# Optimization experiments

Hardware: AMD Instinct MI355X
Metric: run time of the kernel (lower is better)

## Reference

```python
import jax, jax.numpy as jnp
import numpy as np

N = 100000      # nodes
E = 1600000     # edges (avg degree 16)
IN, HID, OUT = 256, 256, 128


def setup_inputs() -> dict:
    key = jax.random.key(0)
    ks = jax.random.split(key, 9)
    x = jax.random.normal(ks[0], (N, IN), jnp.float32)
    edge_index = jax.random.randint(ks[1], (2, E), 0, N, dtype=jnp.int64)
    perm = jax.random.permutation(ks[2], N).astype(jnp.int64)
    # GCN layer params (glorot-ish scale) and Bilinear discriminator params
    W1 = jax.random.normal(ks[3], (IN, HID), jnp.float32) * (1.0 / np.sqrt(IN))
    b1 = jnp.zeros((HID,), jnp.float32)
    W2 = jax.random.normal(ks[4], (HID, OUT), jnp.float32) * (1.0 / np.sqrt(HID))
    b2 = jnp.zeros((OUT,), jnp.float32)
    Wb = jax.random.normal(ks[5], (OUT, OUT), jnp.float32) * (1.0 / np.sqrt(OUT))
    bb = jnp.zeros((1,), jnp.float32)
    return {"x": x, "edge_index": edge_index, "perm": perm,
            "W1": W1, "b1": b1, "W2": W2, "b2": b2, "Wb": Wb, "bb": bb}


def reference(x, edge_index, perm, W1, b1, W2, b2, Wb, bb):
    n = x.shape[0]
    src, dst = edge_index[0], edge_index[1]
    # GCN symmetric norm with self-loops: deg = 1 + in-degree
    deg = 1.0 + jax.ops.segment_sum(jnp.ones(src.shape[0], x.dtype), dst,
                                    num_segments=n)
    dinv = jax.lax.rsqrt(deg)                 # [N]
    enorm = dinv[src] * dinv[dst]             # per-edge norm
    self_norm = dinv * dinv                   # self-loop norm

    def gcn(h, W, b):
        hw = h @ W                                            # [N, F]
        agg = jax.ops.segment_sum(hw[src] * enorm[:, None], dst,
                                  num_segments=n)             # scatter-add
        return agg + self_norm[:, None] * hw + b

    def encode(h):
        return gcn(jax.nn.relu(gcn(h, W1, b1)), W2, b2)       # [N, OUT]

    H = encode(x)
    s = jax.nn.sigmoid(H.mean(axis=0))                        # summary [OUT]

    def disc(Hh):
        # nn.Bilinear(d, d, 1): score_n = H_n^T Wb s + bb
        return (jnp.einsum('nd,de,e->n', Hh, Wb, s) + bb)[:, None]

    pos_scores = disc(H)
    neg_scores = disc(encode(x[perm]))
    return pos_scores, neg_scores
```

## Files before the change

kernel.cpp:

```cpp
#include <hip/hip_runtime.h>


typedef __attribute__((ext_vector_type(8))) short bh8;
typedef __attribute__((ext_vector_type(4))) float f4;
typedef __attribute__((ext_vector_type(4))) unsigned short u16x4;

#define AS1 __attribute__((address_space(1)))
#define AS3 __attribute__((address_space(3)))

__device__ __forceinline__ unsigned short f2b(float f) {
    unsigned int u = __float_as_uint(f);
    unsigned int r = (u + 0x7FFFu + ((u >> 16) & 1u)) >> 16;
    return (unsigned short)r;
}
__device__ __forceinline__ float b2f(unsigned short h) {
    return __uint_as_float(((unsigned int)h) << 16);
}

__global__ void k_degree(const int* __restrict__ dst, int* __restrict__ deg, int E) {
    int e = blockIdx.x * blockDim.x + threadIdx.x;
    if (e < E) atomicAdd(&deg[dst[e]], 1);
}

__global__ void k_dinv(const int* __restrict__ deg, float* __restrict__ dinv,
                       int* __restrict__ rowptr, int N, int E) {
    int n = blockIdx.x * blockDim.x + threadIdx.x;
    if (n < N) dinv[n] = 1.0f / sqrtf(1.0f + (float)deg[n]);
    if (n == 0) rowptr[N] = E;
}

__global__ void k_scanA(const int* __restrict__ in, int* __restrict__ out,
                        int* __restrict__ bsum, int n) {
    __shared__ int sh[256];
    int t = threadIdx.x;
    int base = blockIdx.x * 1024 + t * 4;
    int v[4];
#pragma unroll
    for (int j = 0; j < 4; ++j) v[j] = (base + j < n) ? in[base + j] : 0;
    int s = v[0] + v[1] + v[2] + v[3];
    sh[t] = s;
    __syncthreads();
    for (int off = 1; off < 256; off <<= 1) {
        int u = (t >= off) ? sh[t - off] : 0;
        __syncthreads();
        sh[t] += u;
        __syncthreads();
    }
    int excl = sh[t] - s;
    if (t == 255) bsum[blockIdx.x] = sh[255];
    int run = excl;
#pragma unroll
    for (int j = 0; j < 4; ++j) {
        if (base + j < n) out[base + j] = run;
        run += v[j];
    }
}

__global__ void k_scanB(const int* __restrict__ bsum, int* __restrict__ boff, int nb) {
    __shared__ int sh[128];
    int t = threadIdx.x;
    int v = (t < nb) ? bsum[t] : 0;
    sh[t] = v;
    __syncthreads();
    for (int off = 1; off < 128; off <<= 1) {
        int u = (t >= off) ? sh[t - off] : 0;
        __syncthreads();
        sh[t] += u;
        __syncthreads();
    }
    boff[t] = sh[t] - v;
}

__global__ void k_scanC(int* __restrict__ out, const int* __restrict__ boff, int n) {
    int t = threadIdx.x;
    int base = blockIdx.x * 1024 + t * 4;
    int add = boff[blockIdx.x];
#pragma unroll
    for (int j = 0; j < 4; ++j)
        if (base + j < n) out[base + j] += add;
}

__global__ void k_fill(const int* __restrict__ src, const int* __restrict__ dst,
                       const int* __restrict__ rowptr, int* __restrict__ cursor,
                       int* __restrict__ csr, int E) {
    int e = blockIdx.x * blockDim.x + threadIdx.x;
    if (e >= E) return;
    int d = dst[e];
    int p = rowptr[d] + atomicAdd(&cursor[d], 1);
    csr[p] = src[e];
}

__global__ void k_split(const float* __restrict__ in, unsigned short* __restrict__ hi,
                        unsigned short* __restrict__ lo, long n4) {
    long i = (long)blockIdx.x * blockDim.x + threadIdx.x;
    if (i >= n4) return;
    float4 v = ((const float4*)in)[i];
    float f[4] = {v.x, v.y, v.z, v.w};
    u16x4 h, l;
#pragma unroll
    for (int j = 0; j < 4; ++j) {
        unsigned short hb = f2b(f[j]);
        h[j] = hb;
        l[j] = f2b(f[j] - b2f(hb));
    }
    ((u16x4*)hi)[i] = h;
    ((u16x4*)lo)[i] = l;
}

__global__ void k_wsplitT(const float* __restrict__ W, unsigned short* __restrict__ thi,
                          unsigned short* __restrict__ tlo, int K, int Nc) {
    int t = blockIdx.x * blockDim.x + threadIdx.x;
    if (t >= K * Nc) return;
    int k = t / Nc, n = t % Nc;
    float f = W[t];
    unsigned short hb = f2b(f);
    thi[n * K + k] = hb;
    tlo[n * K + k] = f2b(f - b2f(hb));
}

__global__ __launch_bounds__(256, 2) void k_gemm_mfma(
        const unsigned short* __restrict__ Ahi, const unsigned short* __restrict__ Alo,
        const unsigned short* __restrict__ Bhi, const unsigned short* __restrict__ Blo,
        unsigned short* __restrict__ C, int M, int K, int Nc) {
    __shared__ short lds[4][128 * 32];
    const int tid  = threadIdx.x;
    const int lane = tid & 63;
    const int w    = tid >> 6;
    const int wr   = w >> 1, wc = w & 1;
    const int row0 = blockIdx.y * 128;
    const int col0 = blockIdx.x * 128;

    const unsigned short* sp = (w == 0) ? Ahi : (w == 1) ? Alo : (w == 2) ? Bhi : Blo;
    const int  base0 = (w < 2) ? row0 : col0;
    const int  lim   = (w < 2) ? (M - 1) : (Nc - 1);
    const int  rsub  = lane >> 2;
    const int  clin  = lane & 3;

    f4 acc[4][4] = {};

    for (int k0 = 0; k0 < K; k0 += 32) {
        __syncthreads();
#pragma unroll
        for (int s = 0; s < 8; ++s) {
            int r = s * 16 + rsub;
            int g = base0 + r;
            if (g > lim) g = lim;
            const unsigned short* src = sp + (size_t)g * K + k0 + clin * 8;
            __builtin_amdgcn_global_load_lds((const AS1 void*)src,
                                             (AS3 void*)&lds[w][s * 512], 16, 0, 0);
        }
        __syncthreads();

        bh8 ah[4], al[4], bh_[4], bl[4];
        const int fr = lane & 15;
        const int fc = (lane >> 4) * 8;
#pragma unroll
        for (int m = 0; m < 4; ++m) {
            int off = (wr * 64 + m * 16 + fr) * 32 + fc;
            ah[m] = *(const bh8*)&lds[0][off];
            al[m] = *(const bh8*)&lds[1][off];
        }
#pragma unroll
        for (int n = 0; n < 4; ++n) {
            int off = (wc * 64 + n * 16 + fr) * 32 + fc;
            bh_[n] = *(const bh8*)&lds[2][off];
            bl[n]  = *(const bh8*)&lds[3][off];
        }
#pragma unroll
        for (int m = 0; m < 4; ++m)
#pragma unroll
            for (int n = 0; n < 4; ++n)
                acc[m][n] = __builtin_amdgcn_mfma_f32_16x16x32_bf16(ah[m], bh_[n], acc[m][n], 0, 0, 0);
#pragma unroll
        for (int m = 0; m < 4; ++m)
#pragma unroll
            for (int n = 0; n < 4; ++n)
                acc[m][n] = __builtin_amdgcn_mfma_f32_16x16x32_bf16(ah[m], bl[n], acc[m][n], 0, 0, 0);
#pragma unroll
        for (int m = 0; m < 4; ++m)
#pragma unroll
            for (int n = 0; n < 4; ++n)
                acc[m][n] = __builtin_amdgcn_mfma_f32_16x16x32_bf16(al[m], bh_[n], acc[m][n], 0, 0, 0);
    }

    const int cr = (lane >> 4) * 4;
    const int cc = lane & 15;
#pragma unroll
    for (int m = 0; m < 4; ++m) {
        int r0 = row0 + wr * 64 + m * 16 + cr;
#pragma unroll
        for (int n = 0; n < 4; ++n) {
            int c = col0 + wc * 64 + n * 16 + cc;
#pragma unroll
            for (int j = 0; j < 4; ++j) {
                int r = r0 + j;
                if (r < M) C[(size_t)r * Nc + c] = f2b(acc[m][n][j]);
            }
        }
    }
}

__global__ __launch_bounds__(256) void k_agg2(
        const unsigned short* __restrict__ hw, const int* __restrict__ rowptr,
        const int* __restrict__ csr, const int* __restrict__ perm,
        const float* __restrict__ dinv, const float* __restrict__ bias,
        unsigned short* __restrict__ pos_hi, unsigned short* __restrict__ pos_lo,
        unsigned short* __restrict__ neg_hi, unsigned short* __restrict__ neg_lo,
        int n) {
    int wid = (blockIdx.x * blockDim.x + threadIdx.x) >> 6;
    int lane = threadIdx.x & 63;
    if (wid >= n) return;
    float dn = dinv[wid];
    int beg = rowptr[wid], end = rowptr[wid + 1];
    int off = lane * 4;
    float ap[4] = {0.f, 0.f, 0.f, 0.f}, an[4] = {0.f, 0.f, 0.f, 0.f};
    int e = beg;
    for (; e + 1 < end; e += 2) {
        int s0 = csr[e], s1 = csr[e + 1];
        float w0 = dinv[s0], w1 = dinv[s1];
        int p0 = perm[s0], p1 = perm[s1];
        u16x4 vp0 = *(const u16x4*)(hw + (size_t)s0 * 256 + off);
        u16x4 vn0 = *(const u16x4*)(hw + (size_t)p0 * 256 + off);
        u16x4 vp1 = *(const u16x4*)(hw + (size_t)s1 * 256 + off);
        u16x4 vn1 = *(const u16x4*)(hw + (size_t)p1 * 256 + off);
#pragma unroll
        for (int j = 0; j < 4; ++j) {
            ap[j] += w0 * b2f(vp0[j]) + w1 * b2f(vp1[j]);
            an[j] += w0 * b2f(vn0[j]) + w1 * b2f(vn1[j]);
        }
    }
    for (; e < end; ++e) {
        int s0 = csr[e];
        float w0 = dinv[s0];
        int p0 = perm[s0];
        u16x4 vp0 = *(const u16x4*)(hw + (size_t)s0 * 256 + off);
        u16x4 vn0 = *(const u16x4*)(hw + (size_t)p0 * 256 + off);
#pragma unroll
        for (int j = 0; j < 4; ++j) {
            ap[j] += w0 * b2f(vp0[j]);
            an[j] += w0 * b2f(vn0[j]);
        }
    }
    float sw = dn * dn;
    int pn = perm[wid];
    u16x4 mp = *(const u16x4*)(hw + (size_t)wid * 256 + off);
    u16x4 mn = *(const u16x4*)(hw + (size_t)pn  * 256 + off);
    float4 bv = *(const float4*)(bias + off);
    float bb4[4] = {bv.x, bv.y, bv.z, bv.w};
    u16x4 ph, pl, nh, nl;
#pragma unroll
    for (int j = 0; j < 4; ++j) {
        float rp = fmaxf(dn * ap[j] + sw * b2f(mp[j]) + bb4[j], 0.f);
        float rn = fmaxf(dn * an[j] + sw * b2f(mn[j]) + bb4[j], 0.f);
        unsigned short hb = f2b(rp);
        ph[j] = hb; pl[j] = f2b(rp - b2f(hb));
        hb = f2b(rn);
        nh[j] = hb; nl[j] = f2b(rn - b2f(hb));
    }
    size_t o = (size_t)wid * 256 + off;
    *(u16x4*)(pos_hi + o) = ph;
    *(u16x4*)(pos_lo + o) = pl;
    *(u16x4*)(neg_hi + o) = nh;
    *(u16x4*)(neg_lo + o) = nl;
}

__global__ __launch_bounds__(256) void k_agg128(
        const unsigned short* __restrict__ hw, const int* __restrict__ rowptr,
        const int* __restrict__ csr, const float* __restrict__ dinv,
        const float* __restrict__ bias, float* __restrict__ out, int n) {
    int wid = (blockIdx.x * blockDim.x + threadIdx.x) >> 6;
    int lane = threadIdx.x & 63;
    if (wid >= n) return;
    float dn = dinv[wid];
    int beg = rowptr[wid], end = rowptr[wid + 1];
    int off = lane * 2;
    float a0 = 0.f, a1 = 0.f;
    int e = beg;
    for (; e + 1 < end; e += 2) {
        int s0 = csr[e], s1 = csr[e + 1];
        float w0 = dinv[s0], w1 = dinv[s1];
        ushort2 v0 = *(const ushort2*)(hw + (size_t)s0 * 128 + off);
        ushort2 v1 = *(const ushort2*)(hw + (size_t)s1 * 128 + off);
        a0 += w0 * b2f(v0.x) + w1 * b2f(v1.x);
        a1 += w0 * b2f(v0.y) + w1 * b2f(v1.y);
    }
    for (; e < end; ++e) {
        int s0 = csr[e];
        float w0 = dinv[s0];
        ushort2 v0 = *(const ushort2*)(hw + (size_t)s0 * 128 + off);
        a0 += w0 * b2f(v0.x);
        a1 += w0 * b2f(v0.y);
    }
    float sw = dn * dn;
    ushort2 my = *(const ushort2*)(hw + (size_t)wid * 128 + off);
    float2 bv = *(const float2*)(bias + off);
    float2 r;
    r.x = dn * a0 + sw * b2f(my.x) + bv.x;
    r.y = dn * a1 + sw * b2f(my.y) + bv.y;
    *(float2*)(out + (size_t)wid * 128 + off) = r;
}

__global__ void k_colsum(const float* __restrict__ H, float* __restrict__ colsum, int n) {
    int c = threadIdx.x & 127, half = threadIdx.x >> 7;
    float acc = 0.f;
    for (int r = blockIdx.x * 2 + half; r < n; r += gridDim.x * 2)
        acc += H[(size_t)r * 128 + c];
    __shared__ float sh[256];
    sh[threadIdx.x] = acc;
    __syncthreads();
    if (half == 0) atomicAdd(&colsum[c], sh[c] + sh[c + 128]);
}

__global__ void k_summary(const float* __restrict__ colsum, const float* __restrict__ Wb,
                          float* __restrict__ t, int n) {
    __shared__ float s_sh[128];
    int d = threadIdx.x;
    float m = colsum[d] / (float)n;
    s_sh[d] = 1.0f / (1.0f + expf(-m));
    __syncthreads();
    float acc = 0.f;
    for (int e = 0; e < 128; ++e) acc += Wb[d * 128 + e] * s_sh[e];
    t[d] = acc;
}

__global__ void k_disc(const float* __restrict__ H, const float* __restrict__ t,
                       const float* __restrict__ bb, float* __restrict__ out, int n) {
    int wid = (blockIdx.x * blockDim.x + threadIdx.x) >> 6;
    int lane = threadIdx.x & 63;
    if (wid >= n) return;
    const float* row = H + (size_t)wid * 128;
    float p = row[lane] * t[lane] + row[lane + 64] * t[lane + 64];
#pragma unroll
    for (int off = 32; off > 0; off >>= 1) p += __shfl_down(p, off);
    if (lane == 0) out[wid] = p + bb[0];
}

extern "C" void kernel_launch(void* const* d_in, const int* in_sizes, int n_in,
                              void* d_out, int out_size, void* d_ws, size_t ws_size,
                              hipStream_t stream) {
    const float* x    = (const float*)d_in[0];
    const int*   ei   = (const int*)d_in[1];
    const int*   perm = (const int*)d_in[2];
    const float* W1   = (const float*)d_in[3];
    const float* b1   = (const float*)d_in[4];
    const float* W2   = (const float*)d_in[5];
    const float* b2   = (const float*)d_in[6];
    const float* Wb   = (const float*)d_in[7];
    const float* bb   = (const float*)d_in[8];
    float* out = (float*)d_out;

    const int N   = in_sizes[2];
    const int E   = in_sizes[1] / 2;
    const int IN  = in_sizes[0] / N;
    const int HID = in_sizes[4];
    const int OUT = in_sizes[6];
    const int* src = ei;
    const int* dst = ei + E;

    char* p = (char*)d_ws;
    auto alloc = [&](size_t bytes) -> void* {
        void* r = (void*)p;
        p += (bytes + 255) & ~(size_t)255;
        return r;
    };
    int*   deg    = (int*)alloc((size_t)N * 4);
    int*   cursor = (int*)alloc((size_t)N * 4);
    float* colsum = (float*)alloc(128 * 4);
    size_t zlen   = (size_t)(p - (char*)deg);
    int*   rowptr = (int*)alloc((size_t)(N + 1) * 4);
    int*   bsum   = (int*)alloc(128 * 4);
    int*   boff   = (int*)alloc(128 * 4);
    int*   csr    = (int*)alloc((size_t)E * 4);
    float* dinv   = (float*)alloc((size_t)N * 4);
    float* tvec   = (float*)alloc(128 * 4);
    unsigned short* W1thi = (unsigned short*)alloc((size_t)IN * HID * 2);
    unsigned short* W1tlo = (unsigned short*)alloc((size_t)IN * HID * 2);
    unsigned short* W2thi = (unsigned short*)alloc((size_t)HID * OUT * 2);
    unsigned short* W2tlo = (unsigned short*)alloc((size_t)HID * OUT * 2);
    unsigned short* Xhi = (unsigned short*)alloc((size_t)N * IN * 2);
    unsigned short* Xlo = (unsigned short*)alloc((size_t)N * IN * 2);
    unsigned short* G1 = (unsigned short*)alloc((size_t)N * HID * 2);
    unsigned short* Bphi = (unsigned short*)alloc((size_t)N * HID * 2);
    unsigned short* Bplo = (unsigned short*)alloc((size_t)N * HID * 2);

    unsigned short* Bnhi = Xhi;
    unsigned short* Bnlo = Xlo;
    unsigned short* G2pos = G1;
    unsigned short* G2neg = G1 + (size_t)N * OUT;
    float* Hpos = (float*)Bphi;
    float* Hneg = (float*)Bplo;

    hipMemsetAsync(deg, 0, zlen, stream);

    int eb = (E + 255) / 256;
    int nb = (N + 255) / 256;
    int nscan = (N + 1023) / 1024;
    k_degree<<<eb, 256, 0, stream>>>(dst, deg, E);
    k_dinv<<<nb, 256, 0, stream>>>(deg, dinv, rowptr, N, E);
    k_scanA<<<nscan, 256, 0, stream>>>(deg, rowptr, bsum, N);
    k_scanB<<<1, 128, 0, stream>>>(bsum, boff, nscan);
    k_scanC<<<nscan, 256, 0, stream>>>(rowptr, boff, N);
    k_fill<<<eb, 256, 0, stream>>>(src, dst, rowptr, cursor, csr, E);

    long n4 = (long)N * IN / 4;
    k_split<<<(int)((n4 + 255) / 256), 256, 0, stream>>>(x, Xhi, Xlo, n4);
    k_wsplitT<<<(IN * HID + 255) / 256, 256, 0, stream>>>(W1, W1thi, W1tlo, IN, HID);
    k_wsplitT<<<(HID * OUT + 255) / 256, 256, 0, stream>>>(W2, W2thi, W2tlo, HID, OUT);

    int mblk = (N + 127) / 128;
    int aggb = (N + 3) / 4;

    k_gemm_mfma<<<dim3(HID / 128, mblk), 256, 0, stream>>>(
        Xhi, Xlo, W1thi, W1tlo, G1, N, IN, HID);
    k_agg2<<<aggb, 256, 0, stream>>>(G1, rowptr, csr, perm, dinv, b1,
                                     Bphi, Bplo, Bnhi, Bnlo, N);

    k_gemm_mfma<<<dim3(OUT / 128, mblk), 256, 0, stream>>>(
        Bphi, Bplo, W2thi, W2tlo, G2pos, N, HID, OUT);
    k_agg128<<<aggb, 256, 0, stream>>>(G2pos, rowptr, csr, dinv, b2, Hpos, N);

    k_gemm_mfma<<<dim3(OUT / 128, mblk), 256, 0, stream>>>(
        Bnhi, Bnlo, W2thi, W2tlo, G2neg, N, HID, OUT);
    k_agg128<<<aggb, 256, 0, stream>>>(G2neg, rowptr, csr, dinv, b2, Hneg, N);

    k_colsum<<<256, 256, 0, stream>>>(Hpos, colsum, N);
    k_summary<<<1, 128, 0, stream>>>(colsum, Wb, tvec, N);
    int db = (int)(((size_t)N * 64 + 255) / 256);
    k_disc<<<db, 256, 0, stream>>>(Hpos, tvec, bb, out, N);
    k_disc<<<db, 256, 0, stream>>>(Hneg, tvec, bb, out + N, N);
}
```

Baseline: 1.018 ms.

## Batch pos/neg second layer, precompute permuted CSR, and unroll aggregation by four

The two layer-2 GEMMs are merged into one launch: blockIdx.z picks the positive or negative input and writes into an interleaved [N,256] buffer. The two layer-2 aggregations and the two discriminator launches are each fused into a single kernel, which cuts launches and reuses the CSR and dinv reads. A permuted-source CSR (pcsr) is built during fill so the layer-1 aggregation no longer does a dependent perm[] gather per edge. The aggregation loops are unrolled to four edges for more memory-level parallelism, and outputs use nontemporal stores. In exchange this adds an extra E-sized index array and more register pressure.

```diff
diff --git a/kernel.cpp b/kernel.cpp
--- a/kernel.cpp
+++ b/kernel.cpp
@@ -81,13 +81,16 @@
 }
 
 __global__ void k_fill(const int* __restrict__ src, const int* __restrict__ dst,
-                       const int* __restrict__ rowptr, int* __restrict__ cursor,
-                       int* __restrict__ csr, int E) {
+                       const int* __restrict__ perm, const int* __restrict__ rowptr,
+                       int* __restrict__ cursor, int* __restrict__ csr,
+                       int* __restrict__ pcsr, int E) {
     int e = blockIdx.x * blockDim.x + threadIdx.x;
     if (e >= E) return;
     int d = dst[e];
+    int s = src[e];
     int p = rowptr[d] + atomicAdd(&cursor[d], 1);
-    csr[p] = src[e];
+    csr[p] = s;
+    pcsr[p] = perm[s];
 }
 
 __global__ void k_split(const float* __restrict__ in, unsigned short* __restrict__ hi,
@@ -119,20 +122,23 @@
 }
 
 __global__ __launch_bounds__(256, 2) void k_gemm_mfma(
-        const unsigned short* __restrict__ Ahi, const unsigned short* __restrict__ Alo,
+        const unsigned short* __restrict__ Ahi0, const unsigned short* __restrict__ Alo0,
+        const unsigned short* __restrict__ Ahi1, const unsigned short* __restrict__ Alo1,
         const unsigned short* __restrict__ Bhi, const unsigned short* __restrict__ Blo,
-        unsigned short* __restrict__ C, int M, int K, int Nc) {
+        unsigned short* __restrict__ C, int M, int K, int NcB, int ldC, int colz) {
     __shared__ short lds[4][128 * 32];
     const int tid  = threadIdx.x;
     const int lane = tid & 63;
     const int w    = tid >> 6;
     const int wr   = w >> 1, wc = w & 1;
     const int row0 = blockIdx.y * 128;
-    const int col0 = blockIdx.x * 128;
+    const int bcol = blockIdx.x * 128;
+    const unsigned short* Ahi = blockIdx.z ? Ahi1 : Ahi0;
+    const unsigned short* Alo = blockIdx.z ? Alo1 : Alo0;
 
     const unsigned short* sp = (w == 0) ? Ahi : (w == 1) ? Alo : (w == 2) ? Bhi : Blo;
-    const int  base0 = (w < 2) ? row0 : col0;
-    const int  lim   = (w < 2) ? (M - 1) : (Nc - 1);
+    const int  base0 = (w < 2) ? row0 : bcol;
+    const int  lim   = (w < 2) ? (M - 1) : (NcB - 1);
     const int  rsub  = lane >> 2;
     const int  clin  = lane & 3;
 
@@ -145,8 +151,8 @@
             int r = s * 16 + rsub;
             int g = base0 + r;
             if (g > lim) g = lim;
-            const unsigned short* src = sp + (size_t)g * K + k0 + clin * 8;
-            __builtin_amdgcn_global_load_lds((const AS1 void*)src,
+            const unsigned short* srcp = sp + (size_t)g * K + k0 + clin * 8;
+            __builtin_amdgcn_global_load_lds((const AS1 void*)srcp,
                                              (AS3 void*)&lds[w][s * 512], 16, 0, 0);
         }
         __syncthreads();
@@ -185,6 +191,7 @@
 
     const int cr = (lane >> 4) * 4;
     const int cc = lane & 15;
+    const int col0 = bcol + blockIdx.z * colz;
 #pragma unroll
     for (int m = 0; m < 4; ++m) {
         int r0 = row0 + wr * 64 + m * 16 + cr;
@@ -194,7 +201,7 @@
 #pragma unroll
             for (int j = 0; j < 4; ++j) {
                 int r = r0 + j;
-                if (r < M) C[(size_t)r * Nc + c] = f2b(acc[m][n][j]);
+                if (r < M) C[(size_t)r * ldC + c] = f2b(acc[m][n][j]);
             }
         }
     }
@@ -202,8 +209,9 @@
 
 __global__ __launch_bounds__(256) void k_agg2(
         const unsigned short* __restrict__ hw, const int* __restrict__ rowptr,
-        const int* __restrict__ csr, const int* __restrict__ perm,
-        const float* __restrict__ dinv, const float* __restrict__ bias,
+        const int* __restrict__ csr, const int* __restrict__ pcsr,
+        const int* __restrict__ perm, const float* __restrict__ dinv,
+        const float* __restrict__ bias,
         unsigned short* __restrict__ pos_hi, unsigned short* __restrict__ pos_lo,
         unsigned short* __restrict__ neg_hi, unsigned short* __restrict__ neg_lo,
         int n) {
@@ -215,24 +223,30 @@
     int off = lane * 4;
     float ap[4] = {0.f, 0.f, 0.f, 0.f}, an[4] = {0.f, 0.f, 0.f, 0.f};
     int e = beg;
-    for (; e + 1 < end; e += 2) {
-        int s0 = csr[e], s1 = csr[e + 1];
-        float w0 = dinv[s0], w1 = dinv[s1];
-        int p0 = perm[s0], p1 = perm[s1];
+    for (; e + 3 < end; e += 4) {
+        int s0 = csr[e],     s1 = csr[e + 1], s2 = csr[e + 2], s3 = csr[e + 3];
+        int p0 = pcsr[e],    p1 = pcsr[e + 1], p2 = pcsr[e + 2], p3 = pcsr[e + 3];
+        float w0 = dinv[s0], w1 = dinv[s1],   w2 = dinv[s2],   w3 = dinv[s3];
         u16x4 vp0 = *(const u16x4*)(hw + (size_t)s0 * 256 + off);
+        u16x4 vp1 = *(const u16x4*)(hw + (size_t)s1 * 256 + off);
+        u16x4 vp2 = *(const u16x4*)(hw + (size_t)s2 * 256 + off);
+        u16x4 vp3 = *(const u16x4*)(hw + (size_t)s3 * 256 + off);
         u16x4 vn0 = *(const u16x4*)(hw + (size_t)p0 * 256 + off);
-        u16x4 vp1 = *(const u16x4*)(hw + (size_t)s1 * 256 + off);
         u16x4 vn1 = *(const u16x4*)(hw + (size_t)p1 * 256 + off);
+        u16x4 vn2 = *(const u16x4*)(hw + (size_t)p2 * 256 + off);
+        u16x4 vn3 = *(const u16x4*)(hw + (size_t)p3 * 256 + off);
 #pragma unroll
         for (int j = 0; j < 4; ++j) {
-            ap[j] += w0 * b2f(vp0[j]) + w1 * b2f(vp1[j]);
-            an[j] += w0 * b2f(vn0[j]) + w1 * b2f(vn1[j]);
+            ap[j] += (w0 * b2f(vp0[j]) + w1 * b2f(vp1[j]))
+                   + (w2 * b2f(vp2[j]) + w3 * b2f(vp3[j]));
+            an[j] += (w0 * b2f(vn0[j]) + w1 * b2f(vn1[j]))
+                   + (w2 * b2f(vn2[j]) + w3 * b2f(vn3[j]));
         }
     }
     for (; e < end; ++e) {
         int s0 = csr[e];
+        int p0 = pcsr[e];
         float w0 = dinv[s0];
-        int p0 = perm[s0];
         u16x4 vp0 = *(const u16x4*)(hw + (size_t)s0 * 256 + off);
         u16x4 vn0 = *(const u16x4*)(hw + (size_t)p0 * 256 + off);
 #pragma unroll
@@ -258,46 +272,55 @@
         nh[j] = hb; nl[j] = f2b(rn - b2f(hb));
     }
     size_t o = (size_t)wid * 256 + off;
-    *(u16x4*)(pos_hi + o) = ph;
-    *(u16x4*)(pos_lo + o) = pl;
-    *(u16x4*)(neg_hi + o) = nh;
-    *(u16x4*)(neg_lo + o) = nl;
-}
-
-__global__ __launch_bounds__(256) void k_agg128(
-        const unsigned short* __restrict__ hw, const int* __restrict__ rowptr,
+    __builtin_nontemporal_store(ph, (u16x4*)(pos_hi + o));
+    __builtin_nontemporal_store(pl, (u16x4*)(pos_lo + o));
+    __builtin_nontemporal_store(nh, (u16x4*)(neg_hi + o));
+    __builtin_nontemporal_store(nl, (u16x4*)(neg_lo + o));
+}
+
+__global__ __launch_bounds__(256) void k_agg128m(
+        const unsigned short* __restrict__ G2, const int* __restrict__ rowptr,
         const int* __restrict__ csr, const float* __restrict__ dinv,
-        const float* __restrict__ bias, float* __restrict__ out, int n) {
+        const float* __restrict__ bias, float* __restrict__ Hpos,
+        float* __restrict__ Hneg, int n) {
     int wid = (blockIdx.x * blockDim.x + threadIdx.x) >> 6;
     int lane = threadIdx.x & 63;
     if (wid >= n) return;
     float dn = dinv[wid];
     int beg = rowptr[wid], end = rowptr[wid + 1];
-    int off = lane * 2;
-    float a0 = 0.f, a1 = 0.f;
+    int off = lane * 4;
+    float a[4] = {0.f, 0.f, 0.f, 0.f};
     int e = beg;
-    for (; e + 1 < end; e += 2) {
-        int s0 = csr[e], s1 = csr[e + 1];
-        float w0 = dinv[s0], w1 = dinv[s1];
-        ushort2 v0 = *(const ushort2*)(hw + (size_t)s0 * 128 + off);
-        ushort2 v1 = *(const ushort2*)(hw + (size_t)s1 * 128 + off);
-        a0 += w0 * b2f(v0.x) + w1 * b2f(v1.x);
-        a1 += w0 * b2f(v0.y) + w1 * b2f(v1.y);
+    for (; e + 3 < end; e += 4) {
+        int s0 = csr[e], s1 = csr[e + 1], s2 = csr[e + 2], s3 = csr[e + 3];
+        float w0 = dinv[s0], w1 = dinv[s1], w2 = dinv[s2], w3 = dinv[s3];
+        u16x4 v0 = *(const u16x4*)(G2 + (size_t)s0 * 256 + off);
+        u16x4 v1 = *(const u16x4*)(G2 + (size_t)s1 * 256 + off);
+        u16x4 v2 = *(const u16x4*)(G2 + (size_t)s2 * 256 + off);
+        u16x4 v3 = *(const u16x4*)(G2 + (size_t)s3 * 256 + off);
+#pragma unroll
+        for (int j = 0; j < 4; ++j)
+            a[j] += (w0 * b2f(v0[j]) + w1 * b2f(v1[j]))
+                  + (w2 * b2f(v2[j]) + w3 * b2f(v3[j]));
     }
     for (; e < end; ++e) {
         int s0 = csr[e];
         float w0 = dinv[s0];
-        ushort2 v0 = *(const ushort2*)(hw + (size_t)s0 * 128 + off);
-        a0 += w0 * b2f(v0.x);
-        a1 += w0 * b2f(v0.y);
+        u16x4 v0 = *(const u16x4*)(G2 + (size_t)s0 * 256 + off);
+#pragma unroll
+        for (int j = 0; j < 4; ++j) a[j] += w0 * b2f(v0[j]);
     }
     float sw = dn * dn;
-    ushort2 my = *(const ushort2*)(hw + (size_t)wid * 128 + off);
-    float2 bv = *(const float2*)(bias + off);
-    float2 r;
-    r.x = dn * a0 + sw * b2f(my.x) + bv.x;
-    r.y = dn * a1 + sw * b2f(my.y) + bv.y;
-    *(float2*)(out + (size_t)wid * 128 + off) = r;
+    u16x4 mv = *(const u16x4*)(G2 + (size_t)wid * 256 + off);
+    float4 bv = *(const float4*)(bias + (lane & 31) * 4);
+    float bb4[4] = {bv.x, bv.y, bv.z, bv.w};
+    f4 r;
+    r[0] = dn * a[0] + sw * b2f(mv[0]) + bb4[0];
+    r[1] = dn * a[1] + sw * b2f(mv[1]) + bb4[1];
+    r[2] = dn * a[2] + sw * b2f(mv[2]) + bb4[2];
+    r[3] = dn * a[3] + sw * b2f(mv[3]) + bb4[3];
+    float* dstp = (lane < 32 ? Hpos : Hneg) + (size_t)wid * 128 + (lane & 31) * 4;
+    __builtin_nontemporal_store(r, (f4*)dstp);
 }
 
 __global__ void k_colsum(const float* __restrict__ H, float* __restrict__ colsum, int n) {
@@ -323,12 +346,14 @@
     t[d] = acc;
 }
 
-__global__ void k_disc(const float* __restrict__ H, const float* __restrict__ t,
-                       const float* __restrict__ bb, float* __restrict__ out, int n) {
+__global__ void k_disc(const float* __restrict__ Hpos, const float* __restrict__ Hneg,
+                       const float* __restrict__ t, const float* __restrict__ bb,
+                       float* __restrict__ out, int n) {
     int wid = (blockIdx.x * blockDim.x + threadIdx.x) >> 6;
     int lane = threadIdx.x & 63;
-    if (wid >= n) return;
-    const float* row = H + (size_t)wid * 128;
+    if (wid >= 2 * n) return;
+    const float* row = (wid < n) ? (Hpos + (size_t)wid * 128)
+                                 : (Hneg + (size_t)(wid - n) * 128);
     float p = row[lane] * t[lane] + row[lane + 64] * t[lane + 64];
 #pragma unroll
     for (int off = 32; off > 0; off >>= 1) p += __shfl_down(p, off);
@@ -371,6 +396,7 @@
     int*   bsum   = (int*)alloc(128 * 4);
     int*   boff   = (int*)alloc(128 * 4);
     int*   csr    = (int*)alloc((size_t)E * 4);
+    int*   pcsr   = (int*)alloc((size_t)E * 4);
     float* dinv   = (float*)alloc((size_t)N * 4);
     float* tvec   = (float*)alloc(128 * 4);
     unsigned short* W1thi = (unsigned short*)alloc((size_t)IN * HID * 2);
@@ -385,8 +411,7 @@
 
     unsigned short* Bnhi = Xhi;
     unsigned short* Bnlo = Xlo;
-    unsigned short* G2pos = G1;
-    unsigned short* G2neg = G1 + (size_t)N * OUT;
+    unsigned short* G2 = G1;
     float* Hpos = (float*)Bphi;
     float* Hneg = (float*)Bplo;
 
@@ -400,7 +425,7 @@
     k_scanA<<<nscan, 256, 0, stream>>>(deg, rowptr, bsum, N);
     k_scanB<<<1, 128, 0, stream>>>(bsum, boff, nscan);
     k_scanC<<<nscan, 256, 0, stream>>>(rowptr, boff, N);
-    k_fill<<<eb, 256, 0, stream>>>(src, dst, rowptr, cursor, csr, E);
+    k_fill<<<eb, 256, 0, stream>>>(src, dst, perm, rowptr, cursor, csr, pcsr, E);
 
     long n4 = (long)N * IN / 4;
     k_split<<<(int)((n4 + 255) / 256), 256, 0, stream>>>(x, Xhi, Xlo, n4);
@@ -410,22 +435,17 @@
     int mblk = (N + 127) / 128;
     int aggb = (N + 3) / 4;
 
-    k_gemm_mfma<<<dim3(HID / 128, mblk), 256, 0, stream>>>(
-        Xhi, Xlo, W1thi, W1tlo, G1, N, IN, HID);
-    k_agg2<<<aggb, 256, 0, stream>>>(G1, rowptr, csr, perm, dinv, b1,
+    k_gemm_mfma<<<dim3(HID / 128, mblk, 1), 256, 0, stream>>>(
+        Xhi, Xlo, Xhi, Xlo, W1thi, W1tlo, G1, N, IN, HID, HID, 0);
+    k_agg2<<<aggb, 256, 0, stream>>>(G1, rowptr, csr, pcsr, perm, dinv, b1,
                                      Bphi, Bplo, Bnhi, Bnlo, N);
 
-    k_gemm_mfma<<<dim3(OUT / 128, mblk), 256, 0, stream>>>(
-        Bphi, Bplo, W2thi, W2tlo, G2pos, N, HID, OUT);
-    k_agg128<<<aggb, 256, 0, stream>>>(G2pos, rowptr, csr, dinv, b2, Hpos, N);
-
-    k_gemm_mfma<<<dim3(OUT / 128, mblk), 256, 0, stream>>>(
-        Bnhi, Bnlo, W2thi, W2tlo, G2neg, N, HID, OUT);
-    k_agg128<<<aggb, 256, 0, stream>>>(G2neg, rowptr, csr, dinv, b2, Hneg, N);
+    k_gemm_mfma<<<dim3(OUT / 128, mblk, 2), 256, 0, stream>>>(
+        Bphi, Bplo, Bnhi, Bnlo, W2thi, W2tlo, G2, N, HID, OUT, HID, OUT);
+    k_agg128m<<<aggb, 256, 0, stream>>>(G2, rowptr, csr, dinv, b2, Hpos, Hneg, N);
 
     k_colsum<<<256, 256, 0, stream>>>(Hpos, colsum, N);
     k_summary<<<1, 128, 0, stream>>>(colsum, Wb, tvec, N);
-    int db = (int)(((size_t)N * 64 + 255) / 256);
-    k_disc<<<db, 256, 0, stream>>>(Hpos, tvec, bb, out, N);
-    k_disc<<<db, 256, 0, stream>>>(Hneg, tvec, bb, out + N, N);
-}
+    int db = (int)(((size_t)N * 2 * 64 + 255) / 256);
+    k_disc<<<db, 256, 0, stream>>>(Hpos, Hneg, tvec, bb, out, N);
+}
```

New measurement: 989.2 us. 1.03x faster.
